# Kernel optimization log

Hardware: AMD Instinct MI355X
Metric: run time of the kernel (lower is better)

## Reference

```python
import jax, jax.numpy as jnp
import numpy as np

HEADS = 16

def setup_inputs() -> dict:
    key = jax.random.key(0)
    ks = jax.random.split(key, 7)
    B, Lq, Lkv, D = 2, 1024, 2048, 1024
    return {
        "x_cond": jax.random.normal(ks[0], (B, Lkv, D), dtype=jnp.float32),
        "x_query": jax.random.normal(ks[1], (B, Lq, D), dtype=jnp.float32),
        "tok_emb": jax.random.normal(ks[2], (2, D), dtype=jnp.float32) * 0.02,
        "in_proj_w": jax.random.normal(ks[3], (3 * D, D), dtype=jnp.float32) * (1.0 / np.sqrt(D)),
        "in_proj_b": jax.random.normal(ks[4], (3 * D,), dtype=jnp.float32) * 0.02,
        "out_w": jax.random.normal(ks[5], (D, D), dtype=jnp.float32) * (1.0 / np.sqrt(D)),
        "out_b": jax.random.normal(ks[6], (D,), dtype=jnp.float32) * 0.02,
    }


def reference(x_cond, x_query, tok_emb, in_proj_w, in_proj_b, out_w, out_b):
    B, Lq, D = x_query.shape
    Lkv = x_cond.shape[1]
    H = HEADS
    hd = D // H
    # token-type embedding add: modality 0 -> condition, modality 1 -> query (last input)
    k_in = x_cond + tok_emb[0]    # [B, Lkv, D]
    q_in = x_query + tok_emb[1]   # [B, Lq, D]
    # packed in-projection (PyTorch MultiheadAttention layout: [3D, D])
    wq, wk, wv = jnp.split(in_proj_w, 3, axis=0)
    bq, bk, bv = jnp.split(in_proj_b, 3, axis=0)
    q = (q_in @ wq.T + bq).reshape(B, Lq, H, hd).transpose(0, 2, 1, 3)   # [B,H,Lq,hd]
    k = (k_in @ wk.T + bk).reshape(B, Lkv, H, hd).transpose(0, 2, 1, 3)  # [B,H,Lkv,hd]
    v = (k_in @ wv.T + bv).reshape(B, Lkv, H, hd).transpose(0, 2, 1, 3)  # [B,H,Lkv,hd]
    scale = 1.0 / jnp.sqrt(jnp.asarray(hd, dtype=q.dtype))
    scores = jnp.einsum("bhqd,bhkd->bhqk", q * scale, k)  # [B,H,Lq,Lkv]
    attn = jax.nn.softmax(scores, axis=-1)
    ctx = jnp.einsum("bhqk,bhkd->bhqd", attn, v)           # [B,H,Lq,hd]
    ctx = ctx.transpose(0, 2, 1, 3).reshape(B, Lq, D)
    fused_output = ctx @ out_w.T + out_b                    # [B,Lq,D]
    attn_weights = attn.mean(axis=1)                        # averaged over heads: [B,Lq,Lkv]
    return fused_output, attn_weights
```

## Files before the change

kernel.cpp:

```cpp
#include <hip/hip_runtime.h>
#include <hip/hip_bf16.h>
#include <cstddef>
#include <cstdint>


typedef float  f32x4  __attribute__((ext_vector_type(4)));
typedef short  bf16x8 __attribute__((ext_vector_type(8)));
typedef unsigned short u16x8 __attribute__((ext_vector_type(8)));
typedef __attribute__((address_space(1))) const void gvoid;
typedef __attribute__((address_space(3))) void lvoid;
#define GLD16(g, l) __builtin_amdgcn_global_load_lds((gvoid*)(g), (lvoid*)(l), 16, 0, 0)
#define WAIT_VM0()   asm volatile("s_waitcnt vmcnt(0)" ::: "memory")
#define WAIT_LGKM0() asm volatile("s_waitcnt lgkmcnt(0)" ::: "memory")
#define BAR() __builtin_amdgcn_s_barrier()
#define LOG2E 1.4426950408889634f

static __device__ __forceinline__ unsigned short f2bf(float f) {
    union { float f; unsigned u; } v; v.f = f;
    unsigned r = v.u + 0x7fff + ((v.u >> 16) & 1);
    return (unsigned short)(r >> 16);
}
static __device__ __forceinline__ float bf2f(unsigned short u) {
    union { unsigned u; float f; } v; v.u = (unsigned)u << 16; return v.f;
}

__global__ __launch_bounds__(256)
void conv_bf16(const float* __restrict__ x, const float* __restrict__ tok,
               unsigned short* __restrict__ out, int n8)
{
    int i = blockIdx.x * 256 + threadIdx.x;
    if (i >= n8) return;
    const float4* src = (const float4*)x + (size_t)i * 2;
    float4 a = src[0], b = src[1];
    if (tok) {
        int col = (i * 8) & 1023;
        const float4* tp = (const float4*)(tok + col);
        float4 t0 = tp[0], t1 = tp[1];
        a.x += t0.x; a.y += t0.y; a.z += t0.z; a.w += t0.w;
        b.x += t1.x; b.y += t1.y; b.z += t1.z; b.w += t1.w;
    }
    u16x8 r;
    r[0] = f2bf(a.x); r[1] = f2bf(a.y); r[2] = f2bf(a.z); r[3] = f2bf(a.w);
    r[4] = f2bf(b.x); r[5] = f2bf(b.y); r[6] = f2bf(b.z); r[7] = f2bf(b.w);
    ((u16x8*)out)[i] = r;
}

__global__ __launch_bounds__(256)
void gemm_qkv(const unsigned short* __restrict__ Aq,
              const unsigned short* __restrict__ Ac,
              const unsigned short* __restrict__ W,
              const float* __restrict__ bias,
              unsigned short* __restrict__ Qh,
              unsigned short* __restrict__ Kh,
              unsigned short* __restrict__ Vh)
{
    __shared__ unsigned short As[128 * 64];
    __shared__ unsigned short Bs[128 * 64];
    const int t  = threadIdx.x;
    const int wv = t >> 6, ln = t & 63;
    const int wr = wv >> 1, wc = wv & 1;
    const int lr = ln & 15, lg = ln >> 4;
    const int y = blockIdx.y;

    const unsigned short* A; const unsigned short* Wp; const float* bs;
    unsigned short* Y; int Lshift, m0; float scale;
    if (y < 16)      { A = Aq; m0 = y * 128;        Wp = W;           bs = bias;        Y = Qh; Lshift = 10; scale = 0.125f; }
    else if (y < 48) { A = Ac; m0 = (y - 16) * 128; Wp = W + 1048576; bs = bias + 1024; Y = Kh; Lshift = 11; scale = 1.0f; }
    else             { A = Ac; m0 = (y - 48) * 128; Wp = W + 2097152; bs = bias + 2048; Y = Vh; Lshift = 11; scale = 1.0f; }
    const int n0 = blockIdx.x * 128;

    f32x4 acc[4][4] = {};

    for (int k0 = 0; k0 < 1024; k0 += 64) {
        __syncthreads();
#pragma unroll
        for (int ia = 0; ia < 4; ++ia) {
            int idx = ia * 256 + t;
            int row = idx >> 3, c = idx & 7;
            int sw = (c ^ (row & 7)) * 8;
            GLD16(A  + (size_t)(m0 + row) * 1024 + k0 + sw, As + idx * 8);
            GLD16(Wp + (size_t)(n0 + row) * 1024 + k0 + sw, Bs + idx * 8);
        }
        WAIT_VM0();
        __syncthreads();
#pragma unroll
        for (int ks = 0; ks < 2; ++ks) {
            bf16x8 af[4], bf[4];
#pragma unroll
            for (int i = 0; i < 4; ++i) {
                int rowA = wr * 64 + i * 16 + lr;
                af[i] = *(const bf16x8*)(As + rowA * 64 + (((ks * 4 + lg) ^ (rowA & 7)) * 8));
                int rowB = wc * 64 + i * 16 + lr;
                bf[i] = *(const bf16x8*)(Bs + rowB * 64 + (((ks * 4 + lg) ^ (rowB & 7)) * 8));
            }
#pragma unroll
            for (int i = 0; i < 4; ++i)
#pragma unroll
                for (int j = 0; j < 4; ++j)
                    acc[i][j] = __builtin_amdgcn_mfma_f32_16x16x32_bf16(af[i], bf[j], acc[i][j], 0, 0, 0);
        }
    }

#pragma unroll
    for (int i = 0; i < 4; ++i) {
        int rb = m0 + wr * 64 + i * 16 + lg * 4;
#pragma unroll
        for (int j = 0; j < 4; ++j) {
            int col = n0 + wc * 64 + j * 16 + lr;
            float bv = bs[col];
#pragma unroll
            for (int rr = 0; rr < 4; ++rr) {
                float v = (acc[i][j][rr] + bv) * scale;
                int r = rb + rr;
                int b = r >> Lshift, l = r & ((1 << Lshift) - 1);
                int hh = col >> 6, d = col & 63;
                Y[((((size_t)b * 16 + hh) << Lshift) + l) * 64 + d] = f2bf(v);
            }
        }
    }
}

__global__ __launch_bounds__(256)
void gemm_mfma(const unsigned short* __restrict__ A,
               const unsigned short* __restrict__ W,
               const float* __restrict__ bias,
               float* __restrict__ Y)
{
    __shared__ unsigned short As[128 * 64];
    __shared__ unsigned short Bs[128 * 64];
    const int t  = threadIdx.x;
    const int wv = t >> 6, ln = t & 63;
    const int wr = wv >> 1, wc = wv & 1;
    const int lr = ln & 15, lg = ln >> 4;
    const int m0 = blockIdx.y * 128, n0 = blockIdx.x * 128;

    f32x4 acc[4][4] = {};

    for (int k0 = 0; k0 < 1024; k0 += 64) {
        __syncthreads();
#pragma unroll
        for (int ia = 0; ia < 4; ++ia) {
            int idx = ia * 256 + t;
            int row = idx >> 3, c = idx & 7;
            int sw = (c ^ (row & 7)) * 8;
            GLD16(A + (size_t)(m0 + row) * 1024 + k0 + sw, As + idx * 8);
            GLD16(W + (size_t)(n0 + row) * 1024 + k0 + sw, Bs + idx * 8);
        }
        WAIT_VM0();
        __syncthreads();
#pragma unroll
        for (int ks = 0; ks < 2; ++ks) {
            bf16x8 af[4], bf[4];
#pragma unroll
            for (int i = 0; i < 4; ++i) {
                int rowA = wr * 64 + i * 16 + lr;
                af[i] = *(const bf16x8*)(As + rowA * 64 + (((ks * 4 + lg) ^ (rowA & 7)) * 8));
                int rowB = wc * 64 + i * 16 + lr;
                bf[i] = *(const bf16x8*)(Bs + rowB * 64 + (((ks * 4 + lg) ^ (rowB & 7)) * 8));
            }
#pragma unroll
            for (int i = 0; i < 4; ++i)
#pragma unroll
                for (int j = 0; j < 4; ++j)
                    acc[i][j] = __builtin_amdgcn_mfma_f32_16x16x32_bf16(af[i], bf[j], acc[i][j], 0, 0, 0);
        }
    }

#pragma unroll
    for (int i = 0; i < 4; ++i) {
        int rb = m0 + wr * 64 + i * 16 + lg * 4;
#pragma unroll
        for (int j = 0; j < 4; ++j) {
            int col = n0 + wc * 64 + j * 16 + lr;
            float bv = bias[col];
#pragma unroll
            for (int rr = 0; rr < 4; ++rr)
                Y[(size_t)(rb + rr) * 1024 + col] = acc[i][j][rr] + bv;
        }
    }
}

__global__ __launch_bounds__(256)
void transpose_v(const unsigned short* __restrict__ Vh, unsigned short* __restrict__ Vt)
{
    __shared__ unsigned short L[64 * 72];
    const int t = threadIdx.x;
    const int kt = blockIdx.x;
    const int bh = blockIdx.y;
    const unsigned short* src = Vh + ((size_t)bh * 2048 + kt * 64) * 64;
#pragma unroll
    for (int i = 0; i < 2; ++i) {
        int idx = i * 256 + t;
        int kv = idx >> 3, c = idx & 7;
        *(bf16x8*)(L + kv * 72 + c * 8) = *(const bf16x8*)(src + kv * 64 + c * 8);
    }
    __syncthreads();
#pragma unroll
    for (int i = 0; i < 2; ++i) {
        int idx = i * 256 + t;
        int d = idx >> 3, ck = idx & 7;
        u16x8 r;
#pragma unroll
        for (int j = 0; j < 8; ++j) r[j] = L[(ck * 8 + j) * 72 + d];
        *(u16x8*)(Vt + ((size_t)bh * 64 + d) * 2048 + kt * 64 + ck * 8) = r;
    }
}

__global__ __launch_bounds__(256)
void flash_fwd(const unsigned short* __restrict__ Q,
               const unsigned short* __restrict__ K,
               const unsigned short* __restrict__ Vt,
               unsigned short* __restrict__ pctx,
               float* __restrict__ pm,
               float* __restrict__ pl)
{
    __shared__ unsigned short Ks[2][4096];
    __shared__ unsigned short Vs[2][4096];
    __shared__ unsigned int   Ps32[64 * 32];
    const int t  = threadIdx.x;
    const int wv = t >> 6, ln = t & 63;
    const int lr = ln & 15, lg = ln >> 4;
    const int qt = blockIdx.x, ch = blockIdx.y, bh = blockIdx.z;
    const int q0 = qt * 64;

    const int i0 = t, i1 = 256 + t;
    const int r0 = i0 >> 3, c0 = i0 & 7, sw0 = (c0 ^ (r0 & 7)) * 8;
    const int r1 = i1 >> 3, c1 = i1 & 7, sw1 = (c1 ^ (r1 & 7)) * 8;
    const int l0 = i0 * 8, l1 = i1 * 8;
    const int gk0 = r0 * 64 + sw0,   gk1 = r1 * 64 + sw1;
    const int gv0 = r0 * 2048 + sw0, gv1 = r1 * 2048 + sw1;

    int koff[4];
#pragma unroll
    for (int cf = 0; cf < 4; ++cf)
        koff[cf] = (cf * 16 + lr) * 64 + ((lg ^ (lr & 7)) * 8);
    const int pwB = (wv * 16 + lr) * 32;
    const int pxr = (lr & 7) * 4;
    const int prq0 = (wv * 16 + lr) * 64 + ((lg ^ (lr & 7)) * 8);
    const int prq1 = (wv * 16 + lr) * 64 + (((4 + lg) ^ (lr & 7)) * 8);

    bf16x8 qf[2];
    {
        const unsigned short* qp = Q + ((size_t)bh * 1024 + q0 + wv * 16 + lr) * 64 + lg * 8;
        qf[0] = *(const bf16x8*)qp;
        qf[1] = *(const bf16x8*)(qp + 32);
    }

    f32x4 cacc[4] = {};
    float m2 = -1e30f, lsum = 0.f;

    const unsigned short* kp = K  + ((size_t)bh * 2048 + ch * 1024) * 64;
    const unsigned short* vp = Vt + (size_t)bh * 64 * 2048 + ch * 1024;

    GLD16(kp + gk0, &Ks[0][l0]); GLD16(kp + gk1, &Ks[0][l1]);
    GLD16(vp + gv0, &Vs[0][l0]); GLD16(vp + gv1, &Vs[0][l1]);
    kp += 4096; vp += 64;
    WAIT_VM0();
    BAR();

    int cur = 0;
    for (int tile = 0; tile < 16; ++tile) {
        if (tile < 15) {
            GLD16(kp + gk0, &Ks[cur ^ 1][l0]); GLD16(kp + gk1, &Ks[cur ^ 1][l1]);
            GLD16(vp + gv0, &Vs[cur ^ 1][l0]); GLD16(vp + gv1, &Vs[cur ^ 1][l1]);
            kp += 4096; vp += 64;
        }

        f32x4 sacc[4] = {};
#pragma unroll
        for (int cf = 0; cf < 4; ++cf) {
            bf16x8 kf0 = *(const bf16x8*)(Ks[cur] + koff[cf]);
            sacc[cf] = __builtin_amdgcn_mfma_f32_16x16x32_bf16(kf0, qf[0], sacc[cf], 0, 0, 0);
            bf16x8 kf1 = *(const bf16x8*)(Ks[cur] + (koff[cf] ^ 32));
            sacc[cf] = __builtin_amdgcn_mfma_f32_16x16x32_bf16(kf1, qf[1], sacc[cf], 0, 0, 0);
        }

        float rm;
        {
            float a0 = fmaxf(fmaxf(sacc[0][0], sacc[0][1]), fmaxf(sacc[0][2], sacc[0][3]));
            float a1 = fmaxf(fmaxf(sacc[1][0], sacc[1][1]), fmaxf(sacc[1][2], sacc[1][3]));
            float a2 = fmaxf(fmaxf(sacc[2][0], sacc[2][1]), fmaxf(sacc[2][2], sacc[2][3]));
            float a3 = fmaxf(fmaxf(sacc[3][0], sacc[3][1]), fmaxf(sacc[3][2], sacc[3][3]));
            rm = fmaxf(fmaxf(a0, a1), fmaxf(a2, a3));
        }
        rm = fmaxf(rm, __shfl_xor(rm, 16, 64));
        rm = fmaxf(rm, __shfl_xor(rm, 32, 64));
        rm *= LOG2E;

        if (__any(rm > m2)) {
            float nm = fmaxf(m2, rm);
            float sc = exp2f(m2 - nm);
            m2 = nm;
            lsum *= sc;
            float scB[4];
#pragma unroll
            for (int rr = 0; rr < 4; ++rr)
                scB[rr] = __shfl(sc, (ln & 48) | (lg * 4 + rr), 64);
#pragma unroll
            for (int df = 0; df < 4; ++df)
#pragma unroll
                for (int rr = 0; rr < 4; ++rr) cacc[df][rr] *= scB[rr];
        }

        float p[4][4];
#pragma unroll
        for (int cf = 0; cf < 4; ++cf)
#pragma unroll
            for (int rr = 0; rr < 4; ++rr)
                p[cf][rr] = exp2f(fmaf(sacc[cf][rr], LOG2E, -m2));
#pragma unroll
        for (int cf = 0; cf < 4; ++cf) {
            Ps32[pwB + ((cf * 8 + lg * 2 + 0) ^ pxr)] =
                (unsigned)f2bf(p[cf][0]) | ((unsigned)f2bf(p[cf][1]) << 16);
            Ps32[pwB + ((cf * 8 + lg * 2 + 1) ^ pxr)] =
                (unsigned)f2bf(p[cf][2]) | ((unsigned)f2bf(p[cf][3]) << 16);
        }

        float rs;
        {
            float s0 = (p[0][0] + p[0][1]) + (p[0][2] + p[0][3]);
            float s1 = (p[1][0] + p[1][1]) + (p[1][2] + p[1][3]);
            float s2 = (p[2][0] + p[2][1]) + (p[2][2] + p[2][3]);
            float s3 = (p[3][0] + p[3][1]) + (p[3][2] + p[3][3]);
            rs = (s0 + s1) + (s2 + s3);
        }
        rs += __shfl_xor(rs, 16, 64);
        rs += __shfl_xor(rs, 32, 64);
        lsum += rs;

        WAIT_LGKM0();

#pragma unroll
        for (int kvs = 0; kvs < 2; ++kvs) {
            bf16x8 pf = *(const bf16x8*)((const unsigned short*)Ps32 + (kvs ? prq1 : prq0));
#pragma unroll
            for (int df = 0; df < 4; ++df) {
                bf16x8 vf = *(const bf16x8*)(Vs[cur] + (koff[df] ^ (kvs * 32)));
                cacc[df] = __builtin_amdgcn_mfma_f32_16x16x32_bf16(pf, vf, cacc[df], 0, 0, 0);
            }
        }
        WAIT_VM0();
        BAR();
        cur ^= 1;
    }

    size_t rbase = (size_t)bh * 1024 + q0 + wv * 16;
    unsigned short* pc = pctx + ((size_t)ch * 32768 + rbase) * 64;
#pragma unroll
    for (int df = 0; df < 4; ++df)
#pragma unroll
        for (int rr = 0; rr < 4; ++rr)
            pc[(lg * 4 + rr) * 64 + df * 16 + lr] = f2bf(cacc[df][rr]);
    if (lg == 0) {
        size_t idx = (size_t)ch * 32768 + rbase + lr;
        pm[idx] = m2;
        pl[idx] = lsum;
    }
}

__global__ __launch_bounds__(256)
void combine_flash(const unsigned short* __restrict__ pctx,
                   const float* __restrict__ pm, const float* __restrict__ pl,
                   unsigned short* __restrict__ ctxb,
                   float* __restrict__ m2Out, float* __restrict__ linvOut)
{
    int gid = blockIdx.x * 256 + threadIdx.x;
    int r = gid >> 3, dg = (gid & 7) * 8;
    float m0 = pm[r], m1 = pm[32768 + r];
    float l0 = pl[r], l1 = pl[32768 + r];
    float M = fmaxf(m0, m1);
    float s0 = exp2f(m0 - M), s1 = exp2f(m1 - M);
    float L = fmaf(l0, s0, l1 * s1);
    float linv = 1.f / L;
    float f0 = s0 * linv, f1 = s1 * linv;
    u16x8 a = *(const u16x8*)(pctx + (size_t)r * 64 + dg);
    u16x8 b = *(const u16x8*)(pctx + (size_t)(32768 + r) * 64 + dg);
    u16x8 o;
#pragma unroll
    for (int j = 0; j < 8; ++j)
        o[j] = f2bf(fmaf(bf2f(a[j]), f0, bf2f(b[j]) * f1));
    int bb = r >> 14, h = (r >> 10) & 15, q = r & 1023;
    *(u16x8*)(ctxb + ((size_t)(bb * 1024) + q) * 1024 + h * 64 + dg) = o;
    if (dg == 0) { m2Out[r] = M; linvOut[r] = linv; }
}

__global__ __launch_bounds__(256)
void attn_mean_mfma(const unsigned short* __restrict__ Q,
                    const unsigned short* __restrict__ K,
                    const float* __restrict__ m2In, const float* __restrict__ linvIn,
                    float* __restrict__ attnOut)
{
    __shared__ unsigned short Ks[2][64 * 64];
    const int t  = threadIdx.x;
    const int wv = t >> 6, ln = t & 63;
    const int lr = ln & 15, lg = ln >> 4;
    const int kt = blockIdx.x, qt = blockIdx.y, b = blockIdx.z;
    const int q0 = qt * 64, kv0 = kt * 64;

    const int i0 = t, i1 = 256 + t;
    const int r0 = i0 >> 3, c0 = i0 & 7, sw0 = (c0 ^ (r0 & 7)) * 8;
    const int r1 = i1 >> 3, c1 = i1 & 7, sw1 = (c1 ^ (r1 & 7)) * 8;
    const int l0 = i0 * 8, l1 = i1 * 8;
    const int gk0 = r0 * 64 + sw0, gk1 = r1 * 64 + sw1;

    int koff[4];
#pragma unroll
    for (int cf = 0; cf < 4; ++cf)
        koff[cf] = (cf * 16 + lr) * 64 + ((lg ^ (lr & 7)) * 8);

    const unsigned short* kp = K + ((size_t)(b * 16) * 2048 + kv0) * 64;
    const unsigned short* qp = Q + ((size_t)(b * 16) * 1024 + q0 + wv * 16 + lr) * 64 + lg * 8;
    size_t ridx = (size_t)(b * 16) * 1024 + q0 + wv * 16 + lg * 4;

    float att[4][4] = {};

    GLD16(kp + gk0, &Ks[0][l0]); GLD16(kp + gk1, &Ks[0][l1]);
    kp += 131072;
    WAIT_VM0();
    BAR();

    int cur = 0;
    for (int h = 0; h < 16; ++h) {
        if (h < 15) {
            GLD16(kp + gk0, &Ks[cur ^ 1][l0]); GLD16(kp + gk1, &Ks[cur ^ 1][l1]);
            kp += 131072;
        }
        bf16x8 qf0 = *(const bf16x8*)qp;
        bf16x8 qf1 = *(const bf16x8*)(qp + 32);
        qp += 65536;
        float m2r[4], lir[4];
#pragma unroll
        for (int rr = 0; rr < 4; ++rr) {
            m2r[rr] = m2In[ridx + rr];
            lir[rr] = linvIn[ridx + rr];
        }
        ridx += 1024;

        f32x4 sacc[4] = {};
#pragma unroll
        for (int cf = 0; cf < 4; ++cf) {
            bf16x8 kf0 = *(const bf16x8*)(Ks[cur] + koff[cf]);
            sacc[cf] = __builtin_amdgcn_mfma_f32_16x16x32_bf16(qf0, kf0, sacc[cf], 0, 0, 0);
            bf16x8 kf1 = *(const bf16x8*)(Ks[cur] + (koff[cf] ^ 32));
            sacc[cf] = __builtin_amdgcn_mfma_f32_16x16x32_bf16(qf1, kf1, sacc[cf], 0, 0, 0);
        }
#pragma unroll
        for (int cf = 0; cf < 4; ++cf)
#pragma unroll
            for (int rr = 0; rr < 4; ++rr)
                att[cf][rr] += exp2f(sacc[cf][rr] * LOG2E - m2r[rr]) * lir[rr];

        WAIT_VM0();
        BAR();
        cur ^= 1;
    }

#pragma unroll
    for (int cf = 0; cf < 4; ++cf)
#pragma unroll
        for (int rr = 0; rr < 4; ++rr) {
            int row = q0 + wv * 16 + lg * 4 + rr;
            int col = kv0 + cf * 16 + lr;
            attnOut[((size_t)b * 1024 + row) * 2048 + col] = att[cf][rr] * 0.0625f;
        }
}

extern "C" void kernel_launch(void* const* d_in, const int* in_sizes, int n_in,
                              void* d_out, int out_size, void* d_ws, size_t ws_size,
                              hipStream_t stream)
{
    const float* x_cond  = (const float*)d_in[0];
    const float* x_query = (const float*)d_in[1];
    const float* tok     = (const float*)d_in[2];
    const float* w_in    = (const float*)d_in[3];
    const float* b_in    = (const float*)d_in[4];
    const float* w_out   = (const float*)d_in[5];
    const float* b_out   = (const float*)d_in[6];

    float* fused = (float*)d_out;
    float* attn  = (float*)d_out + 2097152;

    unsigned short* ws = (unsigned short*)d_ws;
    unsigned short* Aq   = ws;
    unsigned short* Ac   = Aq   + 2097152;
    unsigned short* Wb   = Ac   + 4194304;
    unsigned short* Qh   = Wb   + 4194304;
    unsigned short* Kh   = Qh   + 2097152;
    unsigned short* Vh   = Kh   + 4194304;
    unsigned short* Vt   = Vh   + 4194304;
    unsigned short* ctxb = Vt   + 4194304;
    float* m2b = (float*)(ctxb + 2097152);
    float* lib = m2b + 32768;

    unsigned short* pctx = ws;
    float* pmb = (float*)(ws + 4194304);
    float* plb = pmb + 65536;

    conv_bf16<<<1024, 256, 0, stream>>>(x_query, tok + 1024, Aq, 262144);
    conv_bf16<<<2048, 256, 0, stream>>>(x_cond,  tok,        Ac, 524288);
    conv_bf16<<<1536, 256, 0, stream>>>(w_in,  nullptr, Wb,           393216);
    conv_bf16<<< 512, 256, 0, stream>>>(w_out, nullptr, Wb + 3145728, 131072);

    gemm_qkv<<<dim3(8, 80), 256, 0, stream>>>(Aq, Ac, Wb, b_in, Qh, Kh, Vh);

    transpose_v<<<dim3(32, 32), 256, 0, stream>>>(Vh, Vt);

    flash_fwd<<<dim3(16, 2, 32), 256, 0, stream>>>(Qh, Kh, Vt, pctx, pmb, plb);
    combine_flash<<<1024, 256, 0, stream>>>(pctx, pmb, plb, ctxb, m2b, lib);
    attn_mean_mfma<<<dim3(32, 16, 2), 256, 0, stream>>>(Qh, Kh, m2b, lib, attn);

    gemm_mfma<<<dim3(8, 16), 256, 0, stream>>>(ctxb, Wb + 3145728, b_out, fused);
}
```

Baseline: 250.5 us.

## Fuse conversion launches, double-buffer output GEMM, use packed bf16 convert

Merges the four fp32-to-bf16 conversion kernels into one launch that routes each thread to its source by index. Rewrites the output projection GEMM with a 64-row tile, giving twice as many blocks, and double-buffered LDS so the next K tile loads while the current one computes. In the flash kernel it uses the hardware packed bf16 convert instruction for P and reorders the row-max reduction. These cut launch overhead, raise occupancy of the small GEMM, hide load latency and trim ALU work, at the cost of more LDS per block and a change in rounding behaviour from the custom convert.

```diff
diff --git a/kernel.cpp b/kernel.cpp
--- a/kernel.cpp
+++ b/kernel.cpp
@@ -23,18 +23,32 @@
 static __device__ __forceinline__ float bf2f(unsigned short u) {
     union { unsigned u; float f; } v; v.u = (unsigned)u << 16; return v.f;
 }
-
-__global__ __launch_bounds__(256)
-void conv_bf16(const float* __restrict__ x, const float* __restrict__ tok,
-               unsigned short* __restrict__ out, int n8)
+static __device__ __forceinline__ unsigned cvtpk(float lo, float hi) {
+    unsigned r;
+    asm("v_cvt_pk_bf16_f32 %0, %1, %2" : "=v"(r) : "v"(lo), "v"(hi));
+    return r;
+}
+
+__global__ __launch_bounds__(256)
+void conv_all(const float* __restrict__ xq, const float* __restrict__ xc,
+              const float* __restrict__ tok,
+              const float* __restrict__ w_in, const float* __restrict__ w_out,
+              unsigned short* __restrict__ Aq, unsigned short* __restrict__ Ac,
+              unsigned short* __restrict__ Wb)
 {
     int i = blockIdx.x * 256 + threadIdx.x;
-    if (i >= n8) return;
-    const float4* src = (const float4*)x + (size_t)i * 2;
-    float4 a = src[0], b = src[1];
-    if (tok) {
-        int col = (i * 8) & 1023;
-        const float4* tp = (const float4*)(tok + col);
+    const float* src; const float* tokp = nullptr;
+    unsigned short* dst; int off;
+    if (i < 262144)       { src = xq;    tokp = tok + 1024; dst = Aq;            off = i; }
+    else if (i < 786432)  { src = xc;    tokp = tok;        dst = Ac;            off = i - 262144; }
+    else if (i < 1179648) { src = w_in;                     dst = Wb;            off = i - 786432; }
+    else                  { src = w_out;                    dst = Wb + 3145728;  off = i - 1179648; }
+
+    const float4* sp = (const float4*)src + (size_t)off * 2;
+    float4 a = sp[0], b = sp[1];
+    if (tokp) {
+        int col = (off * 8) & 1023;
+        const float4* tp = (const float4*)(tokp + col);
         float4 t0 = tp[0], t1 = tp[1];
         a.x += t0.x; a.y += t0.y; a.z += t0.z; a.w += t0.w;
         b.x += t1.x; b.y += t1.y; b.z += t1.z; b.w += t1.w;
@@ -42,7 +56,7 @@
     u16x8 r;
     r[0] = f2bf(a.x); r[1] = f2bf(a.y); r[2] = f2bf(a.z); r[3] = f2bf(a.w);
     r[4] = f2bf(b.x); r[5] = f2bf(b.y); r[6] = f2bf(b.z); r[7] = f2bf(b.w);
-    ((u16x8*)out)[i] = r;
+    ((u16x8*)dst)[off] = r;
 }
 
 __global__ __launch_bounds__(256)
@@ -121,54 +135,72 @@
 }
 
 __global__ __launch_bounds__(256)
-void gemm_mfma(const unsigned short* __restrict__ A,
-               const unsigned short* __restrict__ W,
-               const float* __restrict__ bias,
-               float* __restrict__ Y)
-{
-    __shared__ unsigned short As[128 * 64];
-    __shared__ unsigned short Bs[128 * 64];
+void gemm_out(const unsigned short* __restrict__ A,
+              const unsigned short* __restrict__ W,
+              const float* __restrict__ bias,
+              float* __restrict__ Y)
+{
+    __shared__ unsigned short As[2][64 * 64];
+    __shared__ unsigned short Bs[2][128 * 64];
     const int t  = threadIdx.x;
     const int wv = t >> 6, ln = t & 63;
     const int wr = wv >> 1, wc = wv & 1;
     const int lr = ln & 15, lg = ln >> 4;
-    const int m0 = blockIdx.y * 128, n0 = blockIdx.x * 128;
-
-    f32x4 acc[4][4] = {};
-
-    for (int k0 = 0; k0 < 1024; k0 += 64) {
-        __syncthreads();
-#pragma unroll
-        for (int ia = 0; ia < 4; ++ia) {
-            int idx = ia * 256 + t;
-            int row = idx >> 3, c = idx & 7;
-            int sw = (c ^ (row & 7)) * 8;
-            GLD16(A + (size_t)(m0 + row) * 1024 + k0 + sw, As + idx * 8);
-            GLD16(W + (size_t)(n0 + row) * 1024 + k0 + sw, Bs + idx * 8);
+    const int m0 = blockIdx.y * 64, n0 = blockIdx.x * 128;
+
+    const int rA0 = (0 * 256 + t) >> 3, cA0 = t & 7, swA0 = (cA0 ^ (rA0 & 7)) * 8;
+    const int rA1 = (1 * 256 + t) >> 3, cA1 = t & 7, swA1 = (cA1 ^ (rA1 & 7)) * 8;
+
+    f32x4 acc[2][4] = {};
+
+#define STAGE_OUT(k0, buf)                                                          \
+    do {                                                                            \
+        GLD16(A + (size_t)(m0 + rA0) * 1024 + (k0) + swA0, &As[buf][(0 * 256 + t) * 8]); \
+        GLD16(A + (size_t)(m0 + rA1) * 1024 + (k0) + swA1, &As[buf][(1 * 256 + t) * 8]); \
+        _Pragma("unroll")                                                           \
+        for (int ia = 0; ia < 4; ++ia) {                                            \
+            int idx = ia * 256 + t;                                                 \
+            int row = idx >> 3, c = idx & 7;                                        \
+            int sw = (c ^ (row & 7)) * 8;                                           \
+            GLD16(W + (size_t)(n0 + row) * 1024 + (k0) + sw, &Bs[buf][idx * 8]);    \
+        }                                                                           \
+    } while (0)
+
+    STAGE_OUT(0, 0);
+    WAIT_VM0();
+    __syncthreads();
+
+    int cur = 0;
+    for (int kt = 0; kt < 16; ++kt) {
+        if (kt < 15) STAGE_OUT((kt + 1) * 64, cur ^ 1);
+#pragma unroll
+        for (int ks = 0; ks < 2; ++ks) {
+            bf16x8 af[2], bf[4];
+#pragma unroll
+            for (int i = 0; i < 2; ++i) {
+                int rowA = wr * 32 + i * 16 + lr;
+                af[i] = *(const bf16x8*)(&As[cur][0] + rowA * 64 + (((ks * 4 + lg) ^ (rowA & 7)) * 8));
+            }
+#pragma unroll
+            for (int j = 0; j < 4; ++j) {
+                int rowB = wc * 64 + j * 16 + lr;
+                bf[j] = *(const bf16x8*)(&Bs[cur][0] + rowB * 64 + (((ks * 4 + lg) ^ (rowB & 7)) * 8));
+            }
+#pragma unroll
+            for (int i = 0; i < 2; ++i)
+#pragma unroll
+                for (int j = 0; j < 4; ++j)
+                    acc[i][j] = __builtin_amdgcn_mfma_f32_16x16x32_bf16(af[i], bf[j], acc[i][j], 0, 0, 0);
         }
         WAIT_VM0();
         __syncthreads();
-#pragma unroll
-        for (int ks = 0; ks < 2; ++ks) {
-            bf16x8 af[4], bf[4];
-#pragma unroll
-            for (int i = 0; i < 4; ++i) {
-                int rowA = wr * 64 + i * 16 + lr;
-                af[i] = *(const bf16x8*)(As + rowA * 64 + (((ks * 4 + lg) ^ (rowA & 7)) * 8));
-                int rowB = wc * 64 + i * 16 + lr;
-                bf[i] = *(const bf16x8*)(Bs + rowB * 64 + (((ks * 4 + lg) ^ (rowB & 7)) * 8));
-            }
-#pragma unroll
-            for (int i = 0; i < 4; ++i)
-#pragma unroll
-                for (int j = 0; j < 4; ++j)
-                    acc[i][j] = __builtin_amdgcn_mfma_f32_16x16x32_bf16(af[i], bf[j], acc[i][j], 0, 0, 0);
-        }
-    }
-
-#pragma unroll
-    for (int i = 0; i < 4; ++i) {
-        int rb = m0 + wr * 64 + i * 16 + lg * 4;
+        cur ^= 1;
+    }
+#undef STAGE_OUT
+
+#pragma unroll
+    for (int i = 0; i < 2; ++i) {
+        int rb = m0 + wr * 32 + i * 16 + lg * 4;
 #pragma unroll
         for (int j = 0; j < 4; ++j) {
             int col = n0 + wc * 64 + j * 16 + lr;
@@ -277,11 +309,12 @@
 
         float rm;
         {
-            float a0 = fmaxf(fmaxf(sacc[0][0], sacc[0][1]), fmaxf(sacc[0][2], sacc[0][3]));
-            float a1 = fmaxf(fmaxf(sacc[1][0], sacc[1][1]), fmaxf(sacc[1][2], sacc[1][3]));
-            float a2 = fmaxf(fmaxf(sacc[2][0], sacc[2][1]), fmaxf(sacc[2][2], sacc[2][3]));
-            float a3 = fmaxf(fmaxf(sacc[3][0], sacc[3][1]), fmaxf(sacc[3][2], sacc[3][3]));
-            rm = fmaxf(fmaxf(a0, a1), fmaxf(a2, a3));
+            float a0 = fmaxf(fmaxf(sacc[0][0], sacc[0][1]), sacc[0][2]);
+            float a1 = fmaxf(fmaxf(sacc[0][3], sacc[1][0]), sacc[1][1]);
+            float a2 = fmaxf(fmaxf(sacc[1][2], sacc[1][3]), sacc[2][0]);
+            float a3 = fmaxf(fmaxf(sacc[2][1], sacc[2][2]), sacc[2][3]);
+            float a4 = fmaxf(fmaxf(sacc[3][0], sacc[3][1]), sacc[3][2]);
+            rm = fmaxf(fmaxf(fmaxf(a0, a1), fmaxf(a2, a3)), fmaxf(a4, sacc[3][3]));
         }
         rm = fmaxf(rm, __shfl_xor(rm, 16, 64));
         rm = fmaxf(rm, __shfl_xor(rm, 32, 64));
@@ -310,10 +343,8 @@
                 p[cf][rr] = exp2f(fmaf(sacc[cf][rr], LOG2E, -m2));
 #pragma unroll
         for (int cf = 0; cf < 4; ++cf) {
-            Ps32[pwB + ((cf * 8 + lg * 2 + 0) ^ pxr)] =
-                (unsigned)f2bf(p[cf][0]) | ((unsigned)f2bf(p[cf][1]) << 16);
-            Ps32[pwB + ((cf * 8 + lg * 2 + 1) ^ pxr)] =
-                (unsigned)f2bf(p[cf][2]) | ((unsigned)f2bf(p[cf][3]) << 16);
+            Ps32[pwB + ((cf * 8 + lg * 2 + 0) ^ pxr)] = cvtpk(p[cf][0], p[cf][1]);
+            Ps32[pwB + ((cf * 8 + lg * 2 + 1) ^ pxr)] = cvtpk(p[cf][2], p[cf][3]);
         }
 
         float rs;
@@ -496,10 +527,7 @@
     float* pmb = (float*)(ws + 4194304);
     float* plb = pmb + 65536;
 
-    conv_bf16<<<1024, 256, 0, stream>>>(x_query, tok + 1024, Aq, 262144);
-    conv_bf16<<<2048, 256, 0, stream>>>(x_cond,  tok,        Ac, 524288);
-    conv_bf16<<<1536, 256, 0, stream>>>(w_in,  nullptr, Wb,           393216);
-    conv_bf16<<< 512, 256, 0, stream>>>(w_out, nullptr, Wb + 3145728, 131072);
+    conv_all<<<5120, 256, 0, stream>>>(x_query, x_cond, tok, w_in, w_out, Aq, Ac, Wb);
 
     gemm_qkv<<<dim3(8, 80), 256, 0, stream>>>(Aq, Ac, Wb, b_in, Qh, Kh, Vh);
 
@@ -509,5 +537,5 @@
     combine_flash<<<1024, 256, 0, stream>>>(pctx, pmb, plb, ctxb, m2b, lib);
     attn_mean_mfma<<<dim3(32, 16, 2), 256, 0, stream>>>(Qh, Kh, m2b, lib, attn);
 
-    gemm_mfma<<<dim3(8, 16), 256, 0, stream>>>(ctxb, Wb + 3145728, b_out, fused);
-}
+    gemm_out<<<dim3(8, 32), 256, 0, stream>>>(ctxb, Wb + 3145728, b_out, fused);
+}
```

Result: faster. 238.7 us (-4.7%).
